# Kernel tuning notes

Measured on AMD Instinct MI355X. Metric: run time of the kernel, lower is better.

The kernel has to match this reference:

```python
import jax, jax.numpy as jnp
import numpy as np

N = 50000
LEAKY_SLOPE = 0.2


def gat_layer(x, src, dst, W, a_src, a_dst, bias, concat):
    """PyG-style GATConv (eval mode, self-loops already in src/dst).
    x: [N, Fin]; W: [Fin, H*C]; a_src, a_dst: [H, C]; bias: [H*C] or [C].
    """
    H, C = a_src.shape
    h = (x @ W).reshape(-1, H, C)                      # [N, H, C]
    alpha_src = jnp.einsum('nhc,hc->nh', h, a_src)      # [N, H]
    alpha_dst = jnp.einsum('nhc,hc->nh', h, a_dst)      # [N, H]
    e = jax.nn.leaky_relu(alpha_src[src] + alpha_dst[dst], LEAKY_SLOPE)  # [E, H]
    # scatter-softmax over incoming edges of each destination node
    m = jax.lax.stop_gradient(jax.ops.segment_max(e, dst, num_segments=N))
    e = jnp.exp(e - m[dst])
    denom = jax.ops.segment_sum(e, dst, num_segments=N)  # [N, H]
    alpha = e / (denom[dst] + 1e-16)                     # [E, H]
    msg = h[src] * alpha[:, :, None]                     # [E, H, C]
    out = jax.ops.segment_sum(msg, dst, num_segments=N)  # [N, H, C]
    out = out.reshape(-1, H * C) if concat else out.mean(axis=1)
    return out + bias


def setup_inputs() -> dict:
    key = jax.random.key(0)
    ks = jax.random.split(key, 10)
    Fin, Hd, Hh = 256, 64, 4
    E = 1600000
    x = jax.random.normal(ks[0], (N, Fin), dtype=jnp.float32)
    edge_index = jax.random.randint(ks[1], (2, E), 0, N, dtype=jnp.int64)
    s = 1.0 / np.sqrt(Fin)
    W1 = jax.random.normal(ks[2], (Fin, Hh * Hd), dtype=jnp.float32) * s
    att_src1 = jax.random.normal(ks[3], (Hh, Hd), dtype=jnp.float32) * (1.0 / np.sqrt(Hd))
    att_dst1 = jax.random.normal(ks[4], (Hh, Hd), dtype=jnp.float32) * (1.0 / np.sqrt(Hd))
    b1 = jnp.zeros((Hh * Hd,), dtype=jnp.float32)
    W2 = jax.random.normal(ks[5], (Hh * Hd, Hd), dtype=jnp.float32) * (1.0 / np.sqrt(Hh * Hd))
    att_src2 = jax.random.normal(ks[6], (1, Hd), dtype=jnp.float32) * (1.0 / np.sqrt(Hd))
    att_dst2 = jax.random.normal(ks[7], (1, Hd), dtype=jnp.float32) * (1.0 / np.sqrt(Hd))
    b2 = jnp.zeros((Hd,), dtype=jnp.float32)
    return {"x": x, "edge_index": edge_index, "W1": W1, "att_src1": att_src1,
            "att_dst1": att_dst1, "b1": b1, "W2": W2, "att_src2": att_src2,
            "att_dst2": att_dst2, "b2": b2}


def reference(x, edge_index, W1, att_src1, att_dst1, b1, W2, att_src2, att_dst2, b2):
    # PyG GATConv adds self-loops by default
    loop = jnp.arange(N, dtype=edge_index.dtype)
    src = jnp.concatenate([edge_index[0], loop])
    dst = jnp.concatenate([edge_index[1], loop])
    h = gat_layer(x, src, dst, W1, att_src1, att_dst1, b1, concat=True)
    h = jax.nn.elu(h)            # dropout is identity in eval mode
    out = gat_layer(h, src, dst, W2, att_src2, att_dst2, b2, concat=False)
    return out
```

## Files before the change

### kernel.cpp

```cpp
#include <hip/hip_runtime.h>


typedef __attribute__((ext_vector_type(8))) short short8;
typedef __attribute__((ext_vector_type(4))) float floatx4;
typedef __attribute__((ext_vector_type(2))) float fx2;

#define FIN 256
#define H1 4
#define CH 64
#define CAP 16384

__device__ __forceinline__ float bf2f(ushort u) {
    union { unsigned int i; float f; } v; v.i = ((unsigned int)u) << 16; return v.f;
}
__device__ __forceinline__ ushort f2bf(float f) {
    union { float f; unsigned int i; } v; v.f = f;
    unsigned int r = v.i + 0x7fffu + ((v.i >> 16) & 1u);
    return (ushort)(r >> 16);
}
__device__ __forceinline__ float load_in(const void* p, int i, int f) {
    return f ? ((const float*)p)[i] : bf2f(((const ushort*)p)[i]);
}
__device__ __forceinline__ int load_idx(const void* p, long long i, int f64) {
    return f64 ? (int)((const long long*)p)[i] : ((const int*)p)[i];
}

__device__ __forceinline__ int pk_off(int row, int k, int KT) {
    return (((row >> 4) * KT + (k >> 5)) << 9) + (((k >> 3) & 3) << 7) +
           ((row & 15) << 3) + (k & 7);
}
__device__ __forceinline__ void pk_dec(int po0, int& row, int& k) {
    int tile = po0 >> 9;
    row = ((tile >> 3) << 4) + ((po0 >> 3) & 15);
    k = ((tile & 7) << 5) + (((po0 >> 7) & 3) << 3);
}

__device__ __forceinline__ float edge_p(float s) {
    s = fmaxf(s, 0.2f * s);
    return __expf(s);
}

__device__ __forceinline__ void accum16(fx2* acc, uint4 v0, uint4 v1,
                                        float p, float& l) {
    l += p;
    fx2 pv = {p, p};
    unsigned w[8] = {v0.x, v0.y, v0.z, v0.w, v1.x, v1.y, v1.z, v1.w};
#pragma unroll
    for (int u = 0; u < 8; ++u) {
        union { unsigned i; float fl; } lo, hi;
        lo.i = w[u] << 16; hi.i = w[u] & 0xffff0000u;
        fx2 c = {lo.fl, hi.fl};
        acc[u] += pv * c;
    }
}

__device__ __forceinline__ void accum8(fx2* acc, uint4 v, float p, float& l) {
    l += p;
    fx2 pv = {p, p};
    unsigned w[4] = {v.x, v.y, v.z, v.w};
#pragma unroll
    for (int u = 0; u < 4; ++u) {
        union { unsigned i; float fl; } lo, hi;
        lo.i = w[u] << 16; hi.i = w[u] & 0xffff0000u;
        fx2 c = {lo.fl, hi.fl};
        acc[u] += pv * c;
    }
}

__global__ __launch_bounds__(256) void probe_kernel(const ushort* __restrict__ x,
                                                    const int* __restrict__ ei,
                                                    int* __restrict__ flags,
                                                    int* __restrict__ bcnt) {
    __shared__ int s_nan, s_odd;
    int t = threadIdx.x;
    bcnt[t] = 0;
    if (t == 0) { s_nan = 0; s_odd = 0; }
    __syncthreads();
    int nanc = 0, oddc = 0;
    for (int i = t; i < 16384; i += 256) {
        ushort u = x[i];
        if (((u >> 7) & 0xFF) == 0xFF) nanc++;
    }
    for (int i = t; i < 2048; i += 256)
        if (ei[2 * i + 1] != 0) oddc++;
    if (nanc) atomicAdd(&s_nan, nanc);
    if (oddc) atomicAdd(&s_odd, oddc);
    __syncthreads();
    if (t == 0) {
        flags[0] = (s_nan >= 2) ? 1 : 0;
        flags[1] = (s_odd == 0) ? 1 : 0;
    }
}

__global__ __launch_bounds__(256) void prep_bucket_kernel(
        const void* __restrict__ x, const void* __restrict__ W1,
        const void* __restrict__ W2, ushort* __restrict__ xb,
        ushort* __restrict__ Wt1, ushort* __restrict__ Wt2,
        const void* __restrict__ ei, int* __restrict__ bcnt,
        unsigned int* __restrict__ buckets,
        int E, int Etot, int Nn, const int* __restrict__ flags,
        int PB_conv, int PB_tr_end) {
    __shared__ int lcnt[256], lbase[256], lcur[256];
    int bid = blockIdx.x, t = threadIdx.x;
    int f = flags[0];
    if (bid < PB_conv) {
        int po0 = bid * 2048 + t * 8;
        int row, k0; pk_dec(po0, row, k0);
        int si = row * FIN + k0;
        if (f) {
            float4 v0 = ((const float4*)x)[si / 4];
            float4 v1 = ((const float4*)x)[si / 4 + 1];
            ushort4 o0, o1;
            o0.x = f2bf(v0.x); o0.y = f2bf(v0.y); o0.z = f2bf(v0.z); o0.w = f2bf(v0.w);
            o1.x = f2bf(v1.x); o1.y = f2bf(v1.y); o1.z = f2bf(v1.z); o1.w = f2bf(v1.w);
            *(ushort4*)(xb + po0) = o0;
            *(ushort4*)(xb + po0 + 4) = o1;
        } else {
            *(uint4*)(xb + po0) = ((const uint4*)x)[si / 8];
        }
        return;
    }
    if (bid < PB_tr_end) {
        int j = (bid - PB_conv) * 256 + t;
        if (j < (FIN * FIN) / 8) {
            int po0 = j * 8;
            int n, k0; pk_dec(po0, n, k0);
            ushort4 o0, o1;
            o0.x = f2bf(load_in(W1, (k0 + 0) * FIN + n, f));
            o0.y = f2bf(load_in(W1, (k0 + 1) * FIN + n, f));
            o0.z = f2bf(load_in(W1, (k0 + 2) * FIN + n, f));
            o0.w = f2bf(load_in(W1, (k0 + 3) * FIN + n, f));
            o1.x = f2bf(load_in(W1, (k0 + 4) * FIN + n, f));
            o1.y = f2bf(load_in(W1, (k0 + 5) * FIN + n, f));
            o1.z = f2bf(load_in(W1, (k0 + 6) * FIN + n, f));
            o1.w = f2bf(load_in(W1, (k0 + 7) * FIN + n, f));
            *(ushort4*)(Wt1 + po0) = o0;
            *(ushort4*)(Wt1 + po0 + 4) = o1;
        } else {
            int po0 = (j - (FIN * FIN) / 8) * 8;
            int n, k0; pk_dec(po0, n, k0);
            ushort4 o0, o1;
            o0.x = f2bf(load_in(W2, (k0 + 0) * CH + n, f));
            o0.y = f2bf(load_in(W2, (k0 + 1) * CH + n, f));
            o0.z = f2bf(load_in(W2, (k0 + 2) * CH + n, f));
            o0.w = f2bf(load_in(W2, (k0 + 3) * CH + n, f));
            o1.x = f2bf(load_in(W2, (k0 + 4) * CH + n, f));
            o1.y = f2bf(load_in(W2, (k0 + 5) * CH + n, f));
            o1.z = f2bf(load_in(W2, (k0 + 6) * CH + n, f));
            o1.w = f2bf(load_in(W2, (k0 + 7) * CH + n, f));
            *(ushort4*)(Wt2 + po0) = o0;
            *(ushort4*)(Wt2 + po0 + 4) = o1;
        }
        return;
    }
    lcnt[t] = 0; lcur[t] = 0;
    __syncthreads();
    int f64 = flags[1];
    int base = (bid - PB_tr_end) * 4096 + t;
    unsigned int val[16]; int bk[16]; bool ok[16];
#pragma unroll
    for (int j = 0; j < 16; ++j) {
        int e = base + j * 256;
        ok[j] = e < Etot;
        bk[j] = 0; val[j] = 0;
        if (ok[j]) {
            int s, d;
            if (e < E) {
                s = load_idx(ei, e, f64);
                d = load_idx(ei, (long long)E + e, f64);
            } else {
                s = d = e - E;
            }
            s = min(max(s, 0), Nn - 1);
            d = min(max(d, 0), Nn - 1);
            bk[j] = d >> 8;
            val[j] = ((unsigned int)s << 8) | (unsigned int)(d & 255);
            atomicAdd(&lcnt[bk[j]], 1);
        }
    }
    __syncthreads();
    if (lcnt[t] > 0) lbase[t] = atomicAdd(&bcnt[t], lcnt[t]);
    __syncthreads();
#pragma unroll
    for (int j = 0; j < 16; ++j) {
        if (ok[j]) {
            int p = lbase[bk[j]] + atomicAdd(&lcur[bk[j]], 1);
            if (p < CAP) buckets[(size_t)bk[j] * CAP + p] = val[j];
        }
    }
}

__device__ __forceinline__ void gemm_core(const ushort* __restrict__ A,
                                          const ushort* __restrict__ Bt,
                                          ushort* __restrict__ C,
                                          int M, int Nc,
                                          const void* __restrict__ aS,
                                          const void* __restrict__ aD,
                                          float* __restrict__ alphaS,
                                          float* __restrict__ alphaD,
                                          int H, int f, int gx, int head,
                                          int planar, int packedA) {
    const int KT = FIN >> 5;
    int tid = threadIdx.x;
    int wave = tid >> 6, lane = tid & 63, quad = lane >> 4, l16 = lane & 15;
    int rbase = gx * 256 + wave * 64;
    int cbase = head * 64;
    int lsub = (quad << 7) + (l16 << 3);
    floatx4 acc[4][4];
#pragma unroll
    for (int i = 0; i < 4; i++)
#pragma unroll
        for (int j = 0; j < 4; j++) acc[i][j] = (floatx4)0.f;

#pragma unroll 2
    for (int kb = 0; kb < FIN; kb += 32) {
        int kt = kb >> 5;
        short8 a[4], b[4];
#pragma unroll
        for (int mt = 0; mt < 4; mt++) {
            if (packedA) {
                int tr = (rbase + mt * 16) >> 4;
                a[mt] = *reinterpret_cast<const short8*>(
                    A + (((size_t)(tr * KT + kt)) << 9) + lsub);
            } else {
                int row = rbase + mt * 16 + l16;
                if (row >= M) row = M - 1;
                a[mt] = *reinterpret_cast<const short8*>(
                    A + (size_t)row * FIN + kb + quad * 8);
            }
        }
#pragma unroll
        for (int nt = 0; nt < 4; nt++) {
            int tc = (cbase + nt * 16) >> 4;
            b[nt] = *reinterpret_cast<const short8*>(
                Bt + (((size_t)(tc * KT + kt)) << 9) + lsub);
        }
#pragma unroll
        for (int mt = 0; mt < 4; mt++)
#pragma unroll
            for (int nt = 0; nt < 4; nt++)
                acc[mt][nt] = __builtin_amdgcn_mfma_f32_16x16x32_bf16(
                    a[mt], b[nt], acc[mt][nt], 0, 0, 0);
    }
    float asv[4], adv[4];
#pragma unroll
    for (int nt = 0; nt < 4; nt++) {
        int col = cbase + nt * 16 + l16;
        asv[nt] = load_in(aS, col, f);
        adv[nt] = load_in(aD, col, f);
    }
#pragma unroll
    for (int mt = 0; mt < 4; mt++) {
#pragma unroll
        for (int r = 0; r < 4; r++) {
            int row = rbase + mt * 16 + quad * 4 + r;
            float ps = 0.f, pd = 0.f;
#pragma unroll
            for (int nt = 0; nt < 4; nt++) {
                float w = acc[mt][nt][r];
                ps += w * asv[nt];
                pd += w * adv[nt];
            }
#pragma unroll
            for (int off = 8; off > 0; off >>= 1) {
                ps += __shfl_xor(ps, off, 16);
                pd += __shfl_xor(pd, off, 16);
            }
            if (row < M) {
                if (l16 == 0) {
                    alphaS[row * H + head] = ps;
                    alphaD[row * H + head] = pd;
                }
#pragma unroll
                for (int nt = 0; nt < 4; nt++) {
                    int col = cbase + nt * 16 + l16;
                    size_t caddr = planar
                        ? ((size_t)(col >> 7) * M + row) * 128 + (col & 127)
                        : (size_t)row * Nc + col;
                    C[caddr] = f2bf(acc[mt][nt][r]);
                }
            }
        }
    }
}

__global__ __launch_bounds__(256) void gemm1_pass2_kernel(
        const ushort* __restrict__ A, const ushort* __restrict__ Bt,
        ushort* __restrict__ C, int M, int Nc,
        const void* __restrict__ aS, const void* __restrict__ aD,
        float* __restrict__ alphaS, float* __restrict__ alphaD,
        const int* __restrict__ flags, int NB, int nbx,
        const int* __restrict__ bcnt, const unsigned int* __restrict__ buckets,
        int* __restrict__ offs, int* __restrict__ csr_src, int Nn) {
    __shared__ int part[256], sc[256], sc4[4][256];
    int bid = blockIdx.x;
    int t = threadIdx.x;
    if (bid >= NB) {
        int g = bid - NB;
        gemm_core(A, Bt, C, M, Nc, aS, aD, alphaS, alphaD, 4, flags[0],
                  g % nbx, g / nbx, 1, 1);
        return;
    }
    int b = bid;
    int w = t >> 6;
    part[t] = bcnt[t];
    sc4[0][t] = 0; sc4[1][t] = 0; sc4[2][t] = 0; sc4[3][t] = 0;
    __syncthreads();
#pragma unroll
    for (int off = 1; off < 256; off <<= 1) {
        int v = (t >= off) ? part[t - off] : 0;
        __syncthreads();
        part[t] += v;
        __syncthreads();
    }
    int basepos = (b == 0) ? 0 : part[b - 1];
    int nEdges = min(bcnt[b], CAP);
    const unsigned int* bk = buckets + (size_t)b * CAP;
    for (int i = t; i < nEdges; i += 256)
        atomicAdd(&sc4[w][bk[i] & 255], 1);
    __syncthreads();
    int c0 = sc4[0][t], c1 = sc4[1][t], c2 = sc4[2][t], c3 = sc4[3][t];
    int mycount = c0 + c1 + c2 + c3;
    sc[t] = mycount;
    __syncthreads();
#pragma unroll
    for (int off = 1; off < 256; off <<= 1) {
        int v = (t >= off) ? sc[t - off] : 0;
        __syncthreads();
        sc[t] += v;
        __syncthreads();
    }
    int excl = sc[t] - mycount;
    int gnode = b * 256 + t;
    if (gnode <= Nn) offs[gnode] = basepos + excl;
    sc4[0][t] = excl;
    sc4[1][t] = excl + c0;
    sc4[2][t] = excl + c0 + c1;
    sc4[3][t] = excl + c0 + c1 + c2;
    __syncthreads();
    for (int i = t; i < nEdges; i += 256) {
        unsigned int v = bk[i];
        int p = atomicAdd(&sc4[w][v & 255], 1);
        csr_src[basepos + p] = (int)(v >> 8);
    }
}

__global__ __launch_bounds__(256) void gemm2_kernel(const ushort* __restrict__ A,
                                                    const ushort* __restrict__ Bt,
                                                    ushort* __restrict__ C,
                                                    int M, int Nc,
                                                    const void* __restrict__ aS,
                                                    const void* __restrict__ aD,
                                                    float* __restrict__ alphaS,
                                                    float* __restrict__ alphaD,
                                                    const int* __restrict__ flags) {
    gemm_core(A, Bt, C, M, Nc, aS, aD, alphaS, alphaD, 1, flags[0],
              blockIdx.x, blockIdx.y, 0, 0);
}

__global__ __launch_bounds__(256) void gat_node1_pass(
        const int* __restrict__ csr_src, const int* __restrict__ offs,
        const float* __restrict__ asrc, const float* __restrict__ adst,
        const ushort* __restrict__ h1p, const void* __restrict__ b1,
        ushort* __restrict__ hmidb, int Nn, const int* __restrict__ flags,
        int plane) {
    int f = flags[0];
    int wave = threadIdx.x >> 6, lane = threadIdx.x & 63;
    int n = blockIdx.x * 4 + wave;
    if (n >= Nn) return;
    int slot = lane >> 3, cg = lane & 7;
    int head = plane * 2 + (cg >> 2);
    float ad = adst[n * H1 + head];
    unsigned rowbase = (unsigned)(plane * Nn) * 128u + (unsigned)cg * 16u;
    int beg = offs[n], end = offs[n + 1];
    fx2 acc[8];
#pragma unroll
    for (int u = 0; u < 8; ++u) acc[u] = (fx2)0.f;
    float l = 0.f;

    int e = beg;
    while (e + 16 <= end) {
        int sa = csr_src[e + slot];
        int sb = csr_src[e + 8 + slot];
        float aa = asrc[sa * H1 + head];
        float ab = asrc[sb * H1 + head];
        const uint4* ra = (const uint4*)(h1p + rowbase + (unsigned)sa * 128u);
        const uint4* rb = (const uint4*)(h1p + rowbase + (unsigned)sb * 128u);
        uint4 va0 = ra[0], va1 = ra[1];
        uint4 vb0 = rb[0], vb1 = rb[1];
        float pa = edge_p(aa + ad);
        float pb = edge_p(ab + ad);
        accum16(acc, va0, va1, pa, l);
        accum16(acc, vb0, vb1, pb, l);
        e += 16;
    }
    if (e < end) {
        int ea = e + slot, eb = e + 8 + slot;
        bool oka = ea < end, okb = eb < end;
        int sa = csr_src[oka ? ea : beg];
        int sb = csr_src[okb ? eb : beg];
        float aa = asrc[sa * H1 + head];
        float ab = asrc[sb * H1 + head];
        const uint4* ra = (const uint4*)(h1p + rowbase + (unsigned)sa * 128u);
        const uint4* rb = (const uint4*)(h1p + rowbase + (unsigned)sb * 128u);
        uint4 va0 = ra[0], va1 = ra[1];
        uint4 vb0 = rb[0], vb1 = rb[1];
        float pa = edge_p(oka ? aa + ad : -1e30f);
        float pb = edge_p(okb ? ab + ad : -1e30f);
        accum16(acc, va0, va1, pa, l);
        accum16(acc, vb0, vb1, pb, l);
    }
#pragma unroll
    for (int off = 8; off <= 32; off <<= 1) {
#pragma unroll
        for (int u = 0; u < 8; ++u) {
            acc[u][0] += __shfl_xor(acc[u][0], off);
            acc[u][1] += __shfl_xor(acc[u][1], off);
        }
        l += __shfl_xor(l, off);
    }
    if (slot == 0) {
        float inv = 1.f / (l + 1e-16f);
        int cb = plane * 128 + cg * 16;
        unsigned ow[8];
#pragma unroll
        for (int u = 0; u < 8; ++u) {
            float o0 = acc[u][0] * inv + load_in(b1, cb + 2 * u, f);
            float o1 = acc[u][1] * inv + load_in(b1, cb + 2 * u + 1, f);
            o0 = o0 > 0.f ? o0 : __expf(o0) - 1.f;
            o1 = o1 > 0.f ? o1 : __expf(o1) - 1.f;
            ow[u] = (unsigned)f2bf(o0) | ((unsigned)f2bf(o1) << 16);
        }
        uint4 st0, st1;
        st0.x = ow[0]; st0.y = ow[1]; st0.z = ow[2]; st0.w = ow[3];
        st1.x = ow[4]; st1.y = ow[5]; st1.z = ow[6]; st1.w = ow[7];
        uint4* dst = (uint4*)(hmidb + (size_t)n * 256 + cb);
        dst[0] = st0; dst[1] = st1;
    }
}

__global__ __launch_bounds__(256) void gat_node2(const int* __restrict__ csr_src,
                                                 const int* __restrict__ offs,
                                                 const float* __restrict__ asrc,
                                                 const float* __restrict__ adst,
                                                 const ushort* __restrict__ h2b,
                                                 const void* __restrict__ b2,
                                                 void* __restrict__ out, int Nn,
                                                 const int* __restrict__ flags) {
    int f = flags[0];
    int wave = threadIdx.x >> 6, lane = threadIdx.x & 63;
    int n = blockIdx.x * 4 + wave;
    if (n >= Nn) return;
    int slot = lane >> 3, cg = lane & 7;
    float ad = adst[n];
    unsigned rowoff = (unsigned)cg * 8u;
    int beg = offs[n], end = offs[n + 1];
    fx2 acc[4];
#pragma unroll
    for (int u = 0; u < 4; ++u) acc[u] = (fx2)0.f;
    float l = 0.f;

    int e = beg;
    while (e + 16 <= end) {
        int sa = csr_src[e + slot];
        int sb = csr_src[e + 8 + slot];
        float aa = asrc[sa];
        float ab = asrc[sb];
        uint4 va = *(const uint4*)(h2b + rowoff + (unsigned)sa * 64u);
        uint4 vb = *(const uint4*)(h2b + rowoff + (unsigned)sb * 64u);
        float pa = edge_p(aa + ad);
        float pb = edge_p(ab + ad);
        accum8(acc, va, pa, l);
        accum8(acc, vb, pb, l);
        e += 16;
    }
    if (e < end) {
        int ea = e + slot, eb = e + 8 + slot;
        bool oka = ea < end, okb = eb < end;
        int sa = csr_src[oka ? ea : beg];
        int sb = csr_src[okb ? eb : beg];
        float aa = asrc[sa];
        float ab = asrc[sb];
        uint4 va = *(const uint4*)(h2b + rowoff + (unsigned)sa * 64u);
        uint4 vb = *(const uint4*)(h2b + rowoff + (unsigned)sb * 64u);
        float pa = edge_p(oka ? aa + ad : -1e30f);
        float pb = edge_p(okb ? ab + ad : -1e30f);
        accum8(acc, va, pa, l);
        accum8(acc, vb, pb, l);
    }
#pragma unroll
    for (int off = 8; off <= 32; off <<= 1) {
#pragma unroll
        for (int u = 0; u < 4; ++u) {
            acc[u][0] += __shfl_xor(acc[u][0], off);
            acc[u][1] += __shfl_xor(acc[u][1], off);
        }
        l += __shfl_xor(l, off);
    }
    if (slot == 0) {
        float inv = 1.f / (l + 1e-16f);
        float o[8];
#pragma unroll
        for (int u = 0; u < 4; ++u) {
            o[2 * u]     = acc[u][0] * inv + load_in(b2, cg * 8 + 2 * u, f);
            o[2 * u + 1] = acc[u][1] * inv + load_in(b2, cg * 8 + 2 * u + 1, f);
        }
        if (f) {
            float* op = (float*)out + (unsigned)n * 64u + (unsigned)cg * 8u;
            float4 s0, s1;
            s0.x = o[0]; s0.y = o[1]; s0.z = o[2]; s0.w = o[3];
            s1.x = o[4]; s1.y = o[5]; s1.z = o[6]; s1.w = o[7];
            *(float4*)op = s0;
            *(float4*)(op + 4) = s1;
        } else {
            uint4 st;
            st.x = (unsigned)f2bf(o[0]) | ((unsigned)f2bf(o[1]) << 16);
            st.y = (unsigned)f2bf(o[2]) | ((unsigned)f2bf(o[3]) << 16);
            st.z = (unsigned)f2bf(o[4]) | ((unsigned)f2bf(o[5]) << 16);
            st.w = (unsigned)f2bf(o[6]) | ((unsigned)f2bf(o[7]) << 16);
            *(uint4*)((ushort*)out + (unsigned)n * 64u + (unsigned)cg * 8u) = st;
        }
    }
}

extern "C" void kernel_launch(void* const* d_in, const int* in_sizes, int n_in,
                              void* d_out, int out_size, void* d_ws, size_t ws_size,
                              hipStream_t stream) {
    const void* x   = d_in[0];
    const void* ei  = d_in[1];
    const void* W1  = d_in[2];
    const void* as1 = d_in[3];
    const void* ad1 = d_in[4];
    const void* b1  = d_in[5];
    const void* W2  = d_in[6];
    const void* as2 = d_in[7];
    const void* ad2 = d_in[8];
    const void* b2  = d_in[9];

    const int Nn = in_sizes[0] / FIN;
    const int E  = in_sizes[1] / 2;
    const int ET = E + Nn;
    const int NB = (Nn + 255) >> 8;

    char* ws = (char*)d_ws;
    size_t off = 0;
    auto alloc = [&](size_t bytes) {
        size_t o = off;
        off += (bytes + 255) & ~(size_t)255;
        return o;
    };
    ushort* xb    = (ushort*)(ws + alloc((size_t)Nn * FIN * 2));
    ushort* h1b   = (ushort*)(ws + alloc((size_t)Nn * FIN * 2));
    ushort* hmidb = (ushort*)(ws + alloc((size_t)Nn * FIN * 2));
    ushort* h2b   = (ushort*)(ws + alloc((size_t)Nn * CH * 2));
    ushort* Wt1   = (ushort*)(ws + alloc((size_t)FIN * FIN * 2));
    ushort* Wt2   = (ushort*)(ws + alloc((size_t)CH * FIN * 2));
    float* as1f   = (float*)(ws + alloc((size_t)Nn * H1 * 4));
    float* ad1f   = (float*)(ws + alloc((size_t)Nn * H1 * 4));
    float* as2f   = (float*)(ws + alloc((size_t)Nn * 4));
    float* ad2f   = (float*)(ws + alloc((size_t)Nn * 4));
    int*   offs   = (int*)(ws + alloc((size_t)(Nn + 1) * 4));
    int*   csr    = (int*)(ws + alloc((size_t)ET * 4));
    unsigned int* buckets = (unsigned int*)(ws + alloc((size_t)256 * CAP * 4));
    int*   bcnt   = (int*)(ws + alloc(256 * 4));
    int*   flags  = (int*)(ws + alloc(256));
    (void)ws_size; (void)n_in; (void)out_size;

    probe_kernel<<<1, 256, 0, stream>>>((const ushort*)x, (const int*)ei, flags, bcnt);

    int PB_conv = (Nn * FIN) / 2048;
    int PB_tr   = (FIN * FIN + CH * FIN) / 2048;
    int PB_bkt  = (ET + 4095) / 4096;
    prep_bucket_kernel<<<PB_conv + PB_tr + PB_bkt, 256, 0, stream>>>(
        x, W1, W2, xb, Wt1, Wt2, ei, bcnt, buckets,
        E, ET, Nn, flags, PB_conv, PB_conv + PB_tr);

    int nbx = (Nn + 255) / 256;
    int g1 = nbx * H1;
    gemm1_pass2_kernel<<<NB + g1, 256, 0, stream>>>(
        xb, Wt1, h1b, Nn, FIN, as1, ad1, as1f, ad1f,
        flags, NB, nbx, bcnt, buckets, offs, csr, Nn);

    gat_node1_pass<<<(Nn + 3) / 4, 256, 0, stream>>>(
        csr, offs, as1f, ad1f, h1b, b1, hmidb, Nn, flags, 0);
    gat_node1_pass<<<(Nn + 3) / 4, 256, 0, stream>>>(
        csr, offs, as1f, ad1f, h1b, b1, hmidb, Nn, flags, 1);

    gemm2_kernel<<<dim3((Nn + 255) / 256, 1), 256, 0, stream>>>(
        hmidb, Wt2, h2b, Nn, CH, as2, ad2, as2f, ad2f, flags);
    gat_node2<<<(Nn + 3) / 4, 256, 0, stream>>>(csr, offs, as2f, ad2f, h2b, b2, d_out, Nn, flags);
}
```

Baseline: 354.5 us.

## Stage GEMM2 A tiles in LDS, swizzle GEMM1 block order, nontemporal CSR loads

GEMM2 no longer reads unpacked row-major A straight from global memory with strided per-lane loads. Each K-step now loads it cooperatively with coalesced 16-byte loads into a padded LDS tile, and the MFMA fragments are read from that tile. GEMM1 blocks are remapped so groups of 8 row tiles run across all 4 heads together, which is meant to improve L2 reuse of A rows. CSR source-index loads in the aggregation kernels become nontemporal so they do not pollute cache. The price is extra syncthreads per K-step in GEMM2 and some idle padded blocks in GEMM1.

```diff
diff --git a/kernel.cpp b/kernel.cpp
--- a/kernel.cpp
+++ b/kernel.cpp
@@ -9,6 +9,7 @@
 #define H1 4
 #define CH 64
 #define CAP 16384
+#define G2S 40
 
 __device__ __forceinline__ float bf2f(ushort u) {
     union { unsigned int i; float f; } v; v.i = ((unsigned int)u) << 16; return v.f;
@@ -193,13 +194,12 @@
 __device__ __forceinline__ void gemm_core(const ushort* __restrict__ A,
                                           const ushort* __restrict__ Bt,
                                           ushort* __restrict__ C,
-                                          int M, int Nc,
+                                          int M,
                                           const void* __restrict__ aS,
                                           const void* __restrict__ aD,
                                           float* __restrict__ alphaS,
                                           float* __restrict__ alphaD,
-                                          int H, int f, int gx, int head,
-                                          int planar, int packedA) {
+                                          int f, int gx, int head) {
     const int KT = FIN >> 5;
     int tid = threadIdx.x;
     int wave = tid >> 6, lane = tid & 63, quad = lane >> 4, l16 = lane & 15;
@@ -218,16 +218,9 @@
         short8 a[4], b[4];
 #pragma unroll
         for (int mt = 0; mt < 4; mt++) {
-            if (packedA) {
-                int tr = (rbase + mt * 16) >> 4;
-                a[mt] = *reinterpret_cast<const short8*>(
-                    A + (((size_t)(tr * KT + kt)) << 9) + lsub);
-            } else {
-                int row = rbase + mt * 16 + l16;
-                if (row >= M) row = M - 1;
-                a[mt] = *reinterpret_cast<const short8*>(
-                    A + (size_t)row * FIN + kb + quad * 8);
-            }
+            int tr = (rbase + mt * 16) >> 4;
+            a[mt] = *reinterpret_cast<const short8*>(
+                A + (((size_t)(tr * KT + kt)) << 9) + lsub);
         }
 #pragma unroll
         for (int nt = 0; nt < 4; nt++) {
@@ -268,15 +261,13 @@
             }
             if (row < M) {
                 if (l16 == 0) {
-                    alphaS[row * H + head] = ps;
-                    alphaD[row * H + head] = pd;
+                    alphaS[row * H1 + head] = ps;
+                    alphaD[row * H1 + head] = pd;
                 }
 #pragma unroll
                 for (int nt = 0; nt < 4; nt++) {
                     int col = cbase + nt * 16 + l16;
-                    size_t caddr = planar
-                        ? ((size_t)(col >> 7) * M + row) * 128 + (col & 127)
-                        : (size_t)row * Nc + col;
+                    size_t caddr = ((size_t)(col >> 7) * M + row) * 128 + (col & 127);
                     C[caddr] = f2bf(acc[mt][nt][r]);
                 }
             }
@@ -286,7 +277,7 @@
 
 __global__ __launch_bounds__(256) void gemm1_pass2_kernel(
         const ushort* __restrict__ A, const ushort* __restrict__ Bt,
-        ushort* __restrict__ C, int M, int Nc,
+        ushort* __restrict__ C, int M,
         const void* __restrict__ aS, const void* __restrict__ aD,
         float* __restrict__ alphaS, float* __restrict__ alphaD,
         const int* __restrict__ flags, int NB, int nbx,
@@ -296,9 +287,11 @@
     int bid = blockIdx.x;
     int t = threadIdx.x;
     if (bid >= NB) {
-        int g = bid - NB;
-        gemm_core(A, Bt, C, M, Nc, aS, aD, alphaS, alphaD, 4, flags[0],
-                  g % nbx, g / nbx, 1, 1);
+        int gg = bid - NB;
+        int r = (gg & 7) | ((gg >> 5) << 3);
+        int h = (gg >> 3) & 3;
+        if (r < nbx)
+            gemm_core(A, Bt, C, M, aS, aD, alphaS, alphaD, flags[0], r, h);
         return;
     }
     int b = bid;
@@ -348,14 +341,90 @@
 __global__ __launch_bounds__(256) void gemm2_kernel(const ushort* __restrict__ A,
                                                     const ushort* __restrict__ Bt,
                                                     ushort* __restrict__ C,
-                                                    int M, int Nc,
+                                                    int M,
                                                     const void* __restrict__ aS,
                                                     const void* __restrict__ aD,
                                                     float* __restrict__ alphaS,
                                                     float* __restrict__ alphaD,
                                                     const int* __restrict__ flags) {
-    gemm_core(A, Bt, C, M, Nc, aS, aD, alphaS, alphaD, 1, flags[0],
-              blockIdx.x, blockIdx.y, 0, 0);
+    __shared__ ushort Asub[256 * G2S];
+    const int KT = FIN >> 5;
+    int t = threadIdx.x;
+    int f = flags[0];
+    int wave = t >> 6, lane = t & 63, quad = lane >> 4, l16 = lane & 15;
+    int rbase = blockIdx.x * 256 + wave * 64;
+    int lsub = (quad << 7) + (l16 << 3);
+    int chunk = t & 3, rr = t >> 2;
+    floatx4 acc[4][4];
+#pragma unroll
+    for (int i = 0; i < 4; i++)
+#pragma unroll
+        for (int j = 0; j < 4; j++) acc[i][j] = (floatx4)0.f;
+
+    for (int kb = 0; kb < FIN; kb += 32) {
+        __syncthreads();
+#pragma unroll
+        for (int rd = 0; rd < 4; ++rd) {
+            int row = blockIdx.x * 256 + rd * 64 + rr;
+            if (row >= M) row = M - 1;
+            uint4 v = *(const uint4*)(A + (size_t)row * FIN + kb + chunk * 8);
+            *(uint4*)(Asub + (rd * 64 + rr) * G2S + chunk * 8) = v;
+        }
+        __syncthreads();
+        int kt = kb >> 5;
+        short8 b[4];
+#pragma unroll
+        for (int nt = 0; nt < 4; nt++) {
+            b[nt] = *reinterpret_cast<const short8*>(
+                Bt + (((size_t)(nt * KT + kt)) << 9) + lsub);
+        }
+#pragma unroll
+        for (int mt = 0; mt < 4; mt++) {
+            short8 a = *reinterpret_cast<const short8*>(
+                Asub + (wave * 64 + mt * 16 + l16) * G2S + quad * 8);
+#pragma unroll
+            for (int nt = 0; nt < 4; nt++)
+                acc[mt][nt] = __builtin_amdgcn_mfma_f32_16x16x32_bf16(
+                    a, b[nt], acc[mt][nt], 0, 0, 0);
+        }
+    }
+    float asv[4], adv[4];
+#pragma unroll
+    for (int nt = 0; nt < 4; nt++) {
+        int col = nt * 16 + l16;
+        asv[nt] = load_in(aS, col, f);
+        adv[nt] = load_in(aD, col, f);
+    }
+#pragma unroll
+    for (int mt = 0; mt < 4; mt++) {
+#pragma unroll
+        for (int r = 0; r < 4; r++) {
+            int row = rbase + mt * 16 + quad * 4 + r;
+            float ps = 0.f, pd = 0.f;
+#pragma unroll
+            for (int nt = 0; nt < 4; nt++) {
+                float w = acc[mt][nt][r];
+                ps += w * asv[nt];
+                pd += w * adv[nt];
+            }
+#pragma unroll
+            for (int off = 8; off > 0; off >>= 1) {
+                ps += __shfl_xor(ps, off, 16);
+                pd += __shfl_xor(pd, off, 16);
+            }
+            if (row < M) {
+                if (l16 == 0) {
+                    alphaS[row] = ps;
+                    alphaD[row] = pd;
+                }
+#pragma unroll
+                for (int nt = 0; nt < 4; nt++) {
+                    int col = nt * 16 + l16;
+                    C[(size_t)row * CH + col] = f2bf(acc[mt][nt][r]);
+                }
+            }
+        }
+    }
 }
 
 __global__ __launch_bounds__(256) void gat_node1_pass(
@@ -380,8 +449,8 @@
 
     int e = beg;
     while (e + 16 <= end) {
-        int sa = csr_src[e + slot];
-        int sb = csr_src[e + 8 + slot];
+        int sa = __builtin_nontemporal_load(csr_src + e + slot);
+        int sb = __builtin_nontemporal_load(csr_src + e + 8 + slot);
         float aa = asrc[sa * H1 + head];
         float ab = asrc[sb * H1 + head];
         const uint4* ra = (const uint4*)(h1p + rowbase + (unsigned)sa * 128u);
@@ -462,8 +531,8 @@
 
     int e = beg;
     while (e + 16 <= end) {
-        int sa = csr_src[e + slot];
-        int sb = csr_src[e + 8 + slot];
+        int sa = __builtin_nontemporal_load(csr_src + e + slot);
+        int sb = __builtin_nontemporal_load(csr_src + e + 8 + slot);
         float aa = asrc[sa];
         float ab = asrc[sb];
         uint4 va = *(const uint4*)(h2b + rowoff + (unsigned)sa * 64u);
@@ -576,9 +645,9 @@
         E, ET, Nn, flags, PB_conv, PB_conv + PB_tr);
 
     int nbx = (Nn + 255) / 256;
-    int g1 = nbx * H1;
-    gemm1_pass2_kernel<<<NB + g1, 256, 0, stream>>>(
-        xb, Wt1, h1b, Nn, FIN, as1, ad1, as1f, ad1f,
+    int ngrp = (nbx + 7) >> 3;
+    gemm1_pass2_kernel<<<NB + ngrp * 32, 256, 0, stream>>>(
+        xb, Wt1, h1b, Nn, as1, ad1, as1f, ad1f,
         flags, NB, nbx, bcnt, buckets, offs, csr, Nn);
 
     gat_node1_pass<<<(Nn + 3) / 4, 256, 0, stream>>>(
@@ -586,7 +655,7 @@
     gat_node1_pass<<<(Nn + 3) / 4, 256, 0, stream>>>(
         csr, offs, as1f, ad1f, h1b, b1, hmidb, Nn, flags, 1);
 
-    gemm2_kernel<<<dim3((Nn + 255) / 256, 1), 256, 0, stream>>>(
-        hmidb, Wt2, h2b, Nn, CH, as2, ad2, as2f, ad2f, flags);
+    gemm2_kernel<<<(Nn + 255) / 256, 256, 0, stream>>>(
+        hmidb, Wt2, h2b, Nn, as2, ad2, as2f, ad2f, flags);
     gat_node2<<<(Nn + 3) / 4, 256, 0, stream>>>(csr, offs, as2f, ad2f, h2b, b2, d_out, Nn, flags);
 }
```

Measured after the change: 358.8 us. Within noise of the previous version (+1.2%).
